# Kernel tuning notes

Measured on AMD Instinct MI355X. Metric: run time of the kernel, lower is better.

## Reference

```python
import jax, jax.numpy as jnp
import numpy as np

THRESH = 0.2  # contact probability threshold from _make_graph default


def setup_inputs() -> dict:
    key = jax.random.key(0)
    ks = jax.random.split(key, 10)
    L, D, K, M = 1024, 640, 32, 64
    S = jax.random.normal(ks[0], (L, D), jnp.float32)
    P = jax.random.uniform(ks[1], (L, L), jnp.float32)
    P = 0.5 * (P + P.T)  # symmetric base-pair probability matrix
    xyz = jax.random.normal(ks[2], (L, 3), jnp.float32) * 10.0  # Angstrom-scale C1' coords
    rbf_mu = jnp.linspace(0.0, 30.0, K).astype(jnp.float32)     # RBF centers over 0-30 A
    rbf_sigma = jax.random.uniform(ks[3], (K,), jnp.float32, 0.5, 2.0)
    W_edge = jax.random.normal(ks[4], (K + 2, M), jnp.float32) * 0.05
    b_edge = jnp.zeros((M,), jnp.float32)
    W_node = jax.random.normal(ks[5], (D, M), jnp.float32) * 0.05
    w_out = jax.random.normal(ks[6], (M,), jnp.float32) * 0.1
    return {"S": S, "P": P, "xyz": xyz, "rbf_mu": rbf_mu, "rbf_sigma": rbf_sigma,
            "W_edge": W_edge, "b_edge": b_edge, "W_node": W_node, "w_out": w_out}


def reference(S, P, xyz, rbf_mu, rbf_sigma, W_edge, b_edge, W_node, w_out):
    """Graph construction (_make_graph) + one SE3-style gated coordinate update.

    Edges: backbone (j == i+1, etype=0, pij=1) and high-prob contacts
    (P[i,j] > THRESH, j > i+2, etype=1, pij=P[i,j]). Edge scalars are
    [etype, pij, rbf(d)] exactly as in _make_graph; edge vectors are
    xyz[j]-xyz[i]. Computed in dense masked form for jit-compatibility.
    """
    L = xyz.shape[0]
    rel = xyz[None, :, :] - xyz[:, None, :]                      # (L,L,3) xyz[j]-xyz[i]
    # safe norm: eps avoids nan grad on zero diagonal (diagonal is masked out anyway)
    d = jnp.sqrt(jnp.sum(rel * rel, axis=-1, keepdims=True) + 1e-12)  # (L,L,1)
    rbf_feat = jnp.exp(-(d - rbf_mu) ** 2 / (2.0 * rbf_sigma ** 2))   # (L,L,K)

    idx = jnp.arange(L)
    backbone = idx[None, :] == idx[:, None] + 1                  # j == i+1
    contact = (P > THRESH) & (idx[None, :] > idx[:, None] + 2)   # skip j <= i+2
    mask = backbone | contact                                    # (L,L)

    etype = contact.astype(S.dtype)                              # 0 backbone, 1 contact
    pij = jnp.where(backbone, jnp.asarray(1.0, S.dtype), P)
    e_scalar = jnp.concatenate([etype[..., None], pij[..., None], rbf_feat], axis=-1)  # (L,L,K+2)

    # gather-compute: message from edge scalars + destination-node scalars
    node_proj = S @ W_node                                       # (L,M)
    msg = jax.nn.relu(jnp.einsum('ijk,km->ijm', e_scalar, W_edge) + b_edge
                      + node_proj[None, :, :])                   # (L,L,M)
    gate = jax.nn.sigmoid(msg @ w_out) * mask.astype(S.dtype)    # (L,L)

    # scatter: equivariant coordinate update, sum of gated edge vectors per node
    xyz_out = xyz + jnp.einsum('ij,ijc->ic', gate, rel)          # (L,3)
    return xyz_out
```

## Files before the change

kernel.cpp:

```cpp
#include <hip/hip_runtime.h>
#include <math.h>

#define LL 1024
#define DD 640
#define KK 32
#define MM 64
#define THRESH 0.2f
#define LOG2E 1.4426950408889634f

#define NPROJ_OFF  0
#define NPROJC_OFF (NPROJ_OFF + LL * MM)
#define WRT_OFF    (NPROJC_OFF + LL * MM)
#define W1_OFF     (WRT_OFF + 1024)
#define EA_OFF     (W1_OFF + MM)
#define EB_OFF     (EA_OFF + KK)
#define EC_OFF     (EB_OFF + KK)
#define XYZ4_OFF   (EC_OFF + KK)

typedef float f32x4_t __attribute__((ext_vector_type(4)));
typedef short bf16x8_t __attribute__((ext_vector_type(8)));

union FragU { unsigned int u[4]; bf16x8_t v; };

#if __has_builtin(__builtin_amdgcn_sqrtf)
#define FSQRT __builtin_amdgcn_sqrtf
#else
#define FSQRT sqrtf
#endif

#if __has_builtin(__builtin_amdgcn_exp2f)
#define EXP2F __builtin_amdgcn_exp2f
#else
#define EXP2F(x) __expf((x) * 0.6931471805599453f)
#endif

__device__ __forceinline__ unsigned int pack_bf(float hi, float lo) {
    return __builtin_amdgcn_perm(__float_as_uint(hi), __float_as_uint(lo), 0x07060302u);
}

__global__ __launch_bounds__(256) void prep_gemm(
    const float* __restrict__ S, const float* __restrict__ xyz,
    const float* __restrict__ rbf_mu, const float* __restrict__ rbf_sigma,
    const float* __restrict__ W_edge, const float* __restrict__ b_edge,
    const float* __restrict__ W_node, float* __restrict__ ws)
{
    const int b = blockIdx.x;
    const int t = threadIdx.x;
    if (b < 64) {
        const int lane = t & 63;
        const int wave = t >> 6;
        const int id   = b * 4 + wave;
        const int r0   = (id >> 2) * 16;
        const int n0   = (id & 3) * 16;
        const int col  = lane & 15;
        const int quad = lane >> 4;

        f32x4_t acc = {0.f, 0.f, 0.f, 0.f};
        const float* arow = S + (size_t)(r0 + col) * DD + quad * 8;
        const float* bcol = W_node + (size_t)(quad * 8) * MM + n0 + col;

        #pragma unroll 2
        for (int ks = 0; ks < 20; ++ks) {
            const float4 a0 = *(const float4*)(arow + ks * 32);
            const float4 a1 = *(const float4*)(arow + ks * 32 + 4);
            FragU A;
            A.u[0] = pack_bf(a0.y, a0.x); A.u[1] = pack_bf(a0.w, a0.z);
            A.u[2] = pack_bf(a1.y, a1.x); A.u[3] = pack_bf(a1.w, a1.z);
            const float* bk = bcol + (size_t)ks * 32 * MM;
            const float b0 = bk[0 * MM], b1 = bk[1 * MM], b2 = bk[2 * MM], b3 = bk[3 * MM];
            const float b4 = bk[4 * MM], b5 = bk[5 * MM], b6 = bk[6 * MM], b7 = bk[7 * MM];
            FragU B;
            B.u[0] = pack_bf(b1, b0); B.u[1] = pack_bf(b3, b2);
            B.u[2] = pack_bf(b5, b4); B.u[3] = pack_bf(b7, b6);
            acc = __builtin_amdgcn_mfma_f32_16x16x32_bf16(A.v, B.v, acc, 0, 0, 0);
        }
        const float bias = b_edge[n0 + col];
        const float w0   = W_edge[n0 + col];
        #pragma unroll
        for (int r = 0; r < 4; ++r) {
            const int row = r0 + quad * 4 + r;
            const float v = acc[r] + bias;
            ws[NPROJ_OFF  + (size_t)row * MM + n0 + col] = v;
            ws[NPROJC_OFF + (size_t)row * MM + n0 + col] = v + w0;
        }
    } else {
        unsigned short* wrt = (unsigned short*)(ws + WRT_OFF);
        if (t < MM) ws[W1_OFF + t] = W_edge[MM + t];
        if (t < KK) {
            const float s  = rbf_sigma[t];
            const float m_ = rbf_mu[t];
            const float inv = 1.0f / (2.0f * s * s);
            ws[EA_OFF + t] = -LOG2E * inv;
            ws[EB_OFF + t] =  2.0f * LOG2E * inv * m_;
            ws[EC_OFF + t] = -LOG2E * inv * m_ * m_;
        }
        for (int idx = t; idx < KK * MM; idx += 256) {
            const int m = idx >> 5, k = idx & 31;
            unsigned int u = __float_as_uint(W_edge[(2 + k) * MM + m]);
            u = (u + 0x7fffu + ((u >> 16) & 1u)) >> 16;
            wrt[idx] = (unsigned short)u;
        }
        for (int n = t; n < LL; n += 256) {
            float4 v;
            v.x = xyz[3 * n + 0]; v.y = xyz[3 * n + 1];
            v.z = xyz[3 * n + 2]; v.w = 0.0f;
            *(float4*)(ws + XYZ4_OFF + 4 * n) = v;
        }
    }
}

__global__ __launch_bounds__(256) void edge_kernel3(
    const float* __restrict__ P, const float* __restrict__ w_out,
    const float* __restrict__ ws, float* __restrict__ out)
{
    const int tid  = threadIdx.x;
    const int lane = tid & 63;
    const int wave = tid >> 6;
    const int quad = lane >> 4;
    const int col  = lane & 15;
    __shared__ float sred[4][3];

    const float* __restrict__ nproj  = ws + NPROJ_OFF;
    const float* __restrict__ nprojc = ws + NPROJC_OFF;
    const float4* __restrict__ xyz4  = (const float4*)(ws + XYZ4_OFF);
    const unsigned short* __restrict__ wrt = (const unsigned short*)(ws + WRT_OFF);

    FragU ar[4];
    float w1r[16], wvr[16];
    float aj[8], bj[8], cj[8];
    #pragma unroll
    for (int mt = 0; mt < 4; ++mt) {
        const uint4 w = *(const uint4*)(wrt + (mt * 16 + col) * KK + quad * 8);
        ar[mt].u[0] = w.x; ar[mt].u[1] = w.y; ar[mt].u[2] = w.z; ar[mt].u[3] = w.w;
        const f32x4_t w1 = *(const f32x4_t*)(ws + W1_OFF + mt * 16 + quad * 4);
        const f32x4_t wo = *(const f32x4_t*)(w_out + mt * 16 + quad * 4);
        #pragma unroll
        for (int r = 0; r < 4; ++r) { w1r[mt * 4 + r] = w1[r]; wvr[mt * 4 + r] = wo[r]; }
    }
    #pragma unroll
    for (int j = 0; j < 8; ++j) {
        aj[j] = ws[EA_OFF + quad * 8 + j];
        bj[j] = ws[EB_OFF + quad * 8 + j];
        cj[j] = ws[EC_OFF + quad * 8 + j];
    }

    const int i = (int)blockIdx.x;
    const float4 xo = xyz4[i];
    const float xi0 = xo.x, xi1 = xo.y, xi2 = xo.z;
    const int len = (LL - 1) - i;
    float ax = 0.f, ay = 0.f, az = 0.f;
    const float* __restrict__ prow = P + (size_t)i * LL;

    for (int base = wave * 64; base < len; base += 256) {
        float pcv[4], dnv[4], q2v[4], dxv[4], dyv[4], dzv[4];
        const float* npr[4];
        float peff[4];
        #pragma unroll
        for (int ct = 0; ct < 4; ++ct) {
            const int jo_n = base + ct * 16 + col;
            int jc = i + 1 + jo_n;
            jc = (jc < LL) ? jc : (LL - 1);
            pcv[ct] = prow[jc];
            const float4 xn = xyz4[jc];
            dxv[ct] = xn.x - xi0; dyv[ct] = xn.y - xi1; dzv[ct] = xn.z - xi2;
            q2v[ct] = fmaf(dxv[ct], dxv[ct],
                      fmaf(dyv[ct], dyv[ct],
                      fmaf(dzv[ct], dzv[ct], 1e-12f)));
            dnv[ct] = FSQRT(q2v[ct]);
            const bool bb = (jo_n == 0);
            peff[ct] = bb ? 1.0f : pcv[ct];
            npr[ct] = (bb ? nproj : nprojc) + (size_t)jc * MM;
        }

        const int jo = base + lane;
        const bool valid = jo < len;
        float rx = dxv[0], ry = dyv[0], rz = dzv[0], p_own = pcv[0];
        rx = (quad == 1) ? dxv[1] : rx; rx = (quad == 2) ? dxv[2] : rx; rx = (quad == 3) ? dxv[3] : rx;
        ry = (quad == 1) ? dyv[1] : ry; ry = (quad == 2) ? dyv[2] : ry; ry = (quad == 3) ? dyv[3] : ry;
        rz = (quad == 1) ? dzv[1] : rz; rz = (quad == 2) ? dzv[2] : rz; rz = (quad == 3) ? dzv[3] : rz;
        p_own = (quad == 1) ? pcv[1] : p_own;
        p_own = (quad == 2) ? pcv[2] : p_own;
        p_own = (quad == 3) ? pcv[3] : p_own;
        const bool msk = valid && ((jo == 0) || ((jo >= 2) && (p_own > THRESH)));

        float e[4][8];
        #pragma unroll
        for (int ct = 0; ct < 4; ++ct)
            #pragma unroll
            for (int j = 0; j < 8; ++j)
                e[ct][j] = EXP2F(fmaf(aj[j], q2v[ct], fmaf(bj[j], dnv[ct], cj[j])));

        FragU bf[4];
        #pragma unroll
        for (int ct = 0; ct < 4; ++ct) {
            bf[ct].u[0] = pack_bf(e[ct][1], e[ct][0]);
            bf[ct].u[1] = pack_bf(e[ct][3], e[ct][2]);
            bf[ct].u[2] = pack_bf(e[ct][5], e[ct][4]);
            bf[ct].u[3] = pack_bf(e[ct][7], e[ct][6]);
        }

        float g[4] = {0.f, 0.f, 0.f, 0.f};
        #pragma unroll
        for (int mt = 0; mt < 4; ++mt) {
            f32x4_t c[4];
            #pragma unroll
            for (int ct = 0; ct < 4; ++ct)
                c[ct] = *(const f32x4_t*)(npr[ct] + mt * 16 + quad * 4);
            #pragma unroll
            for (int ct = 0; ct < 4; ++ct) {
                c[ct][0] = fmaf(peff[ct], w1r[mt*4+0], c[ct][0]);
                c[ct][1] = fmaf(peff[ct], w1r[mt*4+1], c[ct][1]);
                c[ct][2] = fmaf(peff[ct], w1r[mt*4+2], c[ct][2]);
                c[ct][3] = fmaf(peff[ct], w1r[mt*4+3], c[ct][3]);
            }
            #pragma unroll
            for (int ct = 0; ct < 4; ++ct)
                c[ct] = __builtin_amdgcn_mfma_f32_16x16x32_bf16(ar[mt].v, bf[ct].v, c[ct], 0, 0, 0);
            #pragma unroll
            for (int ct = 0; ct < 4; ++ct) {
                g[ct] = fmaf(fmaxf(c[ct][0], 0.f), wvr[mt*4+0], g[ct]);
                g[ct] = fmaf(fmaxf(c[ct][1], 0.f), wvr[mt*4+1], g[ct]);
                g[ct] = fmaf(fmaxf(c[ct][2], 0.f), wvr[mt*4+2], g[ct]);
                g[ct] = fmaf(fmaxf(c[ct][3], 0.f), wvr[mt*4+3], g[ct]);
            }
        }

        #pragma unroll
        for (int ct = 0; ct < 4; ++ct) g[ct] += __shfl_xor(g[ct], 16, 64);
        #pragma unroll
        for (int ct = 0; ct < 4; ++ct) g[ct] += __shfl_xor(g[ct], 32, 64);

        float gd = g[0];
        gd = (quad == 1) ? g[1] : gd;
        gd = (quad == 2) ? g[2] : gd;
        gd = (quad == 3) ? g[3] : gd;
        const float gate = msk ? (1.0f / (1.0f + __expf(-gd))) : 0.0f;
        ax = fmaf(gate, rx, ax);
        ay = fmaf(gate, ry, ay);
        az = fmaf(gate, rz, az);
    }

    #pragma unroll
    for (int off = 32; off > 0; off >>= 1) {
        ax += __shfl_down(ax, off, 64);
        ay += __shfl_down(ay, off, 64);
        az += __shfl_down(az, off, 64);
    }
    if (lane == 0) { sred[wave][0] = ax; sred[wave][1] = ay; sred[wave][2] = az; }
    __syncthreads();
    if (tid == 0) {
        const float tx = (sred[0][0] + sred[1][0]) + (sred[2][0] + sred[3][0]);
        const float ty = (sred[0][1] + sred[1][1]) + (sred[2][1] + sred[3][1]);
        const float tz = (sred[0][2] + sred[1][2]) + (sred[2][2] + sred[3][2]);
        out[i * 3 + 0] = xi0 + tx;
        out[i * 3 + 1] = xi1 + ty;
        out[i * 3 + 2] = xi2 + tz;
    }
}

extern "C" void kernel_launch(void* const* d_in, const int* in_sizes, int n_in,
                              void* d_out, int out_size, void* d_ws, size_t ws_size,
                              hipStream_t stream) {
    const float* S         = (const float*)d_in[0];
    const float* P         = (const float*)d_in[1];
    const float* xyz       = (const float*)d_in[2];
    const float* rbf_mu    = (const float*)d_in[3];
    const float* rbf_sigma = (const float*)d_in[4];
    const float* W_edge    = (const float*)d_in[5];
    const float* b_edge    = (const float*)d_in[6];
    const float* W_node    = (const float*)d_in[7];
    const float* w_out     = (const float*)d_in[8];
    float* out = (float*)d_out;
    float* ws  = (float*)d_ws;

    prep_gemm<<<65, 256, 0, stream>>>(S, xyz, rbf_mu, rbf_sigma,
                                      W_edge, b_edge, W_node, ws);
    edge_kernel3<<<LL, 256, 0, stream>>>(P, w_out, ws, out);
}
```

Measured before the change: 99.44 us.

## Split node-projection GEMM K dimension across waves with shared-memory reduction

The S@W_node projection now uses 256 blocks instead of 64. Each block computes one 16x16 output tile, and its four waves each handle a quarter of the 640-wide reduction before summing the partials through shared memory. This is meant to cut the serial MFMA loop length in the prep kernel and spread the work over more CUs. The cost is an LDS reduction, a barrier, and more blocks to launch.

```diff
diff --git a/kernel.cpp b/kernel.cpp
--- a/kernel.cpp
+++ b/kernel.cpp
@@ -38,7 +38,7 @@
     return __builtin_amdgcn_perm(__float_as_uint(hi), __float_as_uint(lo), 0x07060302u);
 }
 
-__global__ __launch_bounds__(256) void prep_gemm(
+__global__ __launch_bounds__(256) void prep_sk(
     const float* __restrict__ S, const float* __restrict__ xyz,
     const float* __restrict__ rbf_mu, const float* __restrict__ rbf_sigma,
     const float* __restrict__ W_edge, const float* __restrict__ b_edge,
@@ -46,21 +46,21 @@
 {
     const int b = blockIdx.x;
     const int t = threadIdx.x;
-    if (b < 64) {
+    if (b < 256) {
+        __shared__ float red[4][64][4];
         const int lane = t & 63;
         const int wave = t >> 6;
-        const int id   = b * 4 + wave;
-        const int r0   = (id >> 2) * 16;
-        const int n0   = (id & 3) * 16;
+        const int r0   = (b >> 2) * 16;
+        const int n0   = (b & 3) * 16;
         const int col  = lane & 15;
         const int quad = lane >> 4;
 
         f32x4_t acc = {0.f, 0.f, 0.f, 0.f};
-        const float* arow = S + (size_t)(r0 + col) * DD + quad * 8;
-        const float* bcol = W_node + (size_t)(quad * 8) * MM + n0 + col;
-
-        #pragma unroll 2
-        for (int ks = 0; ks < 20; ++ks) {
+        const float* arow = S + (size_t)(r0 + col) * DD + wave * 160 + quad * 8;
+        const float* bcol = W_node + (size_t)(wave * 160 + quad * 8) * MM + n0 + col;
+
+        #pragma unroll
+        for (int ks = 0; ks < 5; ++ks) {
             const float4 a0 = *(const float4*)(arow + ks * 32);
             const float4 a1 = *(const float4*)(arow + ks * 32 + 4);
             FragU A;
@@ -74,15 +74,20 @@
             B.u[2] = pack_bf(b5, b4); B.u[3] = pack_bf(b7, b6);
             acc = __builtin_amdgcn_mfma_f32_16x16x32_bf16(A.v, B.v, acc, 0, 0, 0);
         }
-        const float bias = b_edge[n0 + col];
-        const float w0   = W_edge[n0 + col];
-        #pragma unroll
-        for (int r = 0; r < 4; ++r) {
-            const int row = r0 + quad * 4 + r;
-            const float v = acc[r] + bias;
-            ws[NPROJ_OFF  + (size_t)row * MM + n0 + col] = v;
-            ws[NPROJC_OFF + (size_t)row * MM + n0 + col] = v + w0;
-        }
+        red[wave][lane][0] = acc[0];
+        red[wave][lane][1] = acc[1];
+        red[wave][lane][2] = acc[2];
+        red[wave][lane][3] = acc[3];
+        __syncthreads();
+        const int lr  = t & 63;
+        const int reg = t >> 6;
+        const float v = (red[0][lr][reg] + red[1][lr][reg])
+                      + (red[2][lr][reg] + red[3][lr][reg]);
+        const int row = r0 + (lr >> 4) * 4 + reg;
+        const int cc  = n0 + (lr & 15);
+        const float vb = v + b_edge[cc];
+        ws[NPROJ_OFF  + (size_t)row * MM + cc] = vb;
+        ws[NPROJC_OFF + (size_t)row * MM + cc] = vb + W_edge[cc];
     } else {
         unsigned short* wrt = (unsigned short*)(ws + WRT_OFF);
         if (t < MM) ws[W1_OFF + t] = W_edge[MM + t];
@@ -273,7 +278,7 @@
     float* out = (float*)d_out;
     float* ws  = (float*)d_ws;
 
-    prep_gemm<<<65, 256, 0, stream>>>(S, xyz, rbf_mu, rbf_sigma,
-                                      W_edge, b_edge, W_node, ws);
+    prep_sk<<<257, 256, 0, stream>>>(S, xyz, rbf_mu, rbf_sigma,
+                                     W_edge, b_edge, W_node, ws);
     edge_kernel3<<<LL, 256, 0, stream>>>(P, w_out, ws, out);
 }
```

Result: no change. 97.50 us (-2.0%).
